# Kernel optimization log

Hardware: AMD Instinct MI355X
Metric: run time of the kernel (lower is better)

Reference implementation:

```python
import jax, jax.numpy as jnp
import numpy as np

TOKENS, D_IN, D_OUT, RANK = 32768, 1024, 1024, 16
SCALE1 = 8.0 / RANK   # alpha=8, rank=16
SCALE2 = 16.0 / RANK  # alpha=16, rank=16


def setup_inputs() -> dict:
    key = jax.random.key(0)
    ks = jax.random.split(key, 7)
    inv = 1.0 / np.sqrt(D_IN)
    return {
        "x": jax.random.normal(ks[0], (TOKENS, D_IN), jnp.float32),
        "W": jax.random.normal(ks[1], (D_OUT, D_IN), jnp.float32) * inv,
        "b": jax.random.normal(ks[2], (D_OUT,), jnp.float32) * 0.01,
        "A1": jax.random.normal(ks[3], (RANK, D_IN), jnp.float32) * inv,
        "B1": jax.random.normal(ks[4], (D_OUT, RANK), jnp.float32) * 0.01,
        "A2": jax.random.normal(ks[5], (RANK, D_IN), jnp.float32) * inv,
        "B2": jax.random.normal(ks[6], (D_OUT, RANK), jnp.float32) * 0.01,
    }


def reference(x, W, b, A1, B1, A2, B2):
    # base linear: [T, D_in] @ [D_in, D_out] + b
    out = jnp.einsum("ti,oi->to", x, W) + b
    # LoRA adapter 1: scale * (x @ A1^T) @ B1^T   (dropout=Identity in eval)
    out = out + SCALE1 * jnp.einsum("tr,or->to", jnp.einsum("ti,ri->tr", x, A1), B1)
    # LoRA adapter 2
    out = out + SCALE2 * jnp.einsum("tr,or->to", jnp.einsum("ti,ri->tr", x, A2), B2)
    return out
```

## Files before the change

### kernel.cpp

```cpp
#include <hip/hip_runtime.h>

#define TOKENS 32768
#define DIN 1024
#define DOUT 1024
#define RANK 16
#define SCALE1 0.5f
#define SCALE2 1.0f

#define BM 128
#define BN 128
#define BK 32

typedef __bf16 bf16x8 __attribute__((ext_vector_type(8)));
typedef float f32x4 __attribute__((ext_vector_type(4)));

__device__ __forceinline__ void load_lds16(const void* gptr, void* lptr) {
    __builtin_amdgcn_global_load_lds(
        (__attribute__((address_space(1))) void*)gptr,
        (__attribute__((address_space(3))) void*)lptr, 16, 0, 0);
}

__global__ void weff_kernel(const float* __restrict__ W, const float* __restrict__ A1,
                            const float* __restrict__ B1, const float* __restrict__ A2,
                            const float* __restrict__ B2, __bf16* __restrict__ Weff) {
    int idx = blockIdx.x * blockDim.x + threadIdx.x;
    int o = idx >> 10;
    int i = idx & 1023;
    float s1 = 0.f, s2 = 0.f;
#pragma unroll
    for (int r = 0; r < RANK; ++r) {
        s1 += B1[o * RANK + r] * A1[r * DIN + i];
        s2 += B2[o * RANK + r] * A2[r * DIN + i];
    }
    Weff[idx] = (__bf16)(W[idx] + SCALE1 * s1 + SCALE2 * s2);
}

__global__ void cvt_x_kernel(const float* __restrict__ x, __bf16* __restrict__ xb) {
    int i = (blockIdx.x * blockDim.x + threadIdx.x) * 8;
    float4 a = *(const float4*)(x + i);
    float4 b = *(const float4*)(x + i + 4);
    bf16x8 v;
    v[0] = (__bf16)a.x; v[1] = (__bf16)a.y; v[2] = (__bf16)a.z; v[3] = (__bf16)a.w;
    v[4] = (__bf16)b.x; v[5] = (__bf16)b.y; v[6] = (__bf16)b.z; v[7] = (__bf16)b.w;
    *(bf16x8*)(xb + i) = v;
}

__global__ __launch_bounds__(256) void gemm_bt_kernel(
    const __bf16* __restrict__ A,
    const __bf16* __restrict__ Bw,
    const float* __restrict__ bias, float* __restrict__ C) {
    __shared__ alignas(16) __bf16 lsA[2][BM * BK];
    __shared__ alignas(16) __bf16 lsB[2][BN * BK];

    const int tid = threadIdx.x;
    const int wave = tid >> 6;
    const int lane = tid & 63;

    const int l = blockIdx.x;
    const int xcd = l & 7;
    const int s = l >> 3;
    const int m0 = (xcd * 32 + (s >> 3)) * BM;
    const int n0 = (s & 7) * BN;

    const int wm = wave >> 1;
    const int wn = wave & 1;

    const int lrow = lane >> 2;
    const int lcol = ((lane & 3) ^ ((lane >> 3) & 3)) * 8;

    const __bf16* gA = A + (size_t)(m0 + wave * 32 + lrow) * DIN + lcol;
    const __bf16* gB = Bw + (size_t)(n0 + wave * 32 + lrow) * DIN + lcol;
    const int so0 = (wave * 32) * BK;
    const int so1 = so0 + 16 * BK;

    f32x4 acc[4][4];
#pragma unroll
    for (int i = 0; i < 4; ++i)
#pragma unroll
        for (int j = 0; j < 4; ++j) acc[i][j] = f32x4{0.f, 0.f, 0.f, 0.f};

    const int fr = lane & 15;
    const int fsw = ((lane >> 4) ^ ((lane >> 1) & 3)) * 8;

    load_lds16(gA, &lsA[0][so0]);
    load_lds16(gA + 16 * DIN, &lsA[0][so1]);
    load_lds16(gB, &lsB[0][so0]);
    load_lds16(gB + 16 * DIN, &lsB[0][so1]);

    int cur = 0;
    for (int k0 = 0; k0 < DIN; k0 += BK) {
        __syncthreads();

        if (k0 + BK < DIN) {
            const int kn = k0 + BK;
            load_lds16(gA + kn, &lsA[cur ^ 1][so0]);
            load_lds16(gA + kn + 16 * DIN, &lsA[cur ^ 1][so1]);
            load_lds16(gB + kn, &lsB[cur ^ 1][so0]);
            load_lds16(gB + kn + 16 * DIN, &lsB[cur ^ 1][so1]);
        }

        bf16x8 af[4], bfv[4];
#pragma unroll
        for (int t = 0; t < 4; ++t) {
            af[t] = *(const bf16x8*)&lsA[cur][(wm * 64 + t * 16 + fr) * BK + fsw];
            bfv[t] = *(const bf16x8*)&lsB[cur][(wn * 64 + t * 16 + fr) * BK + fsw];
        }
#pragma unroll
        for (int mt = 0; mt < 4; ++mt)
#pragma unroll
            for (int nt = 0; nt < 4; ++nt)
                acc[mt][nt] = __builtin_amdgcn_mfma_f32_16x16x32_bf16(
                    af[mt], bfv[nt], acc[mt][nt], 0, 0, 0);
        cur ^= 1;
    }

    const int rbase = (lane >> 4) * 4;
#pragma unroll
    for (int nt = 0; nt < 4; ++nt) {
        const int n = n0 + wn * 64 + nt * 16 + fr;
        const float bv = bias[n];
#pragma unroll
        for (int mt = 0; mt < 4; ++mt) {
            const int m = m0 + wm * 64 + mt * 16 + rbase;
            float* cp = C + (size_t)m * DOUT + n;
#pragma unroll
            for (int r = 0; r < 4; ++r) cp[(size_t)r * DOUT] = acc[mt][nt][r] + bv;
        }
    }
}

extern "C" void kernel_launch(void* const* d_in, const int* in_sizes, int n_in,
                              void* d_out, int out_size, void* d_ws, size_t ws_size,
                              hipStream_t stream) {
    const float* x  = (const float*)d_in[0];
    const float* W  = (const float*)d_in[1];
    const float* b  = (const float*)d_in[2];
    const float* A1 = (const float*)d_in[3];
    const float* B1 = (const float*)d_in[4];
    const float* A2 = (const float*)d_in[5];
    const float* B2 = (const float*)d_in[6];
    float* out = (float*)d_out;

    __bf16* xb   = (__bf16*)d_ws;
    __bf16* Weff = (__bf16*)((char*)d_ws + (size_t)TOKENS * DIN * sizeof(__bf16));

    cvt_x_kernel<<<TOKENS * DIN / (256 * 8), 256, 0, stream>>>(x, xb);
    weff_kernel<<<DOUT * DIN / 256, 256, 0, stream>>>(W, A1, B1, A2, B2, Weff);
    gemm_bt_kernel<<<(TOKENS / BM) * (DOUT / BN), 256, 0, stream>>>(xb, Weff, b, out);
}
```

Before: 330.0 us.

## Use 256x256x64 tiles with 8 waves and phased MFMA/load interleaving

Grows the GEMM block tile to 256x256 with BK=64 and 512 threads (8 waves, each owning a 128x64 sub-tile). The K loop is split into four phases that interleave global-to-LDS prefetch of the next tile with MFMA work, using explicit barriers, setprio and a new 8-column XOR swizzle. The aim is more operand reuse per LDS byte, fewer barriers per FLOP and better overlap of loads with compute. In exchange it uses more registers and LDS per block, which may limit occupancy, and leaves fewer blocks in the grid.

```diff
diff --git a/kernel.cpp b/kernel.cpp
--- a/kernel.cpp
+++ b/kernel.cpp
@@ -7,9 +7,10 @@
 #define SCALE1 0.5f
 #define SCALE2 1.0f
 
-#define BM 128
-#define BN 128
-#define BK 32
+#define BM 256
+#define BN 256
+#define BK 64
+#define KTILES (DIN / BK)
 
 typedef __bf16 bf16x8 __attribute__((ext_vector_type(8)));
 typedef float f32x4 __attribute__((ext_vector_type(4)));
@@ -45,12 +46,12 @@
     *(bf16x8*)(xb + i) = v;
 }
 
-__global__ __launch_bounds__(256) void gemm_bt_kernel(
+__global__ __launch_bounds__(512, 2) void gemm_bt_kernel(
     const __bf16* __restrict__ A,
     const __bf16* __restrict__ Bw,
     const float* __restrict__ bias, float* __restrict__ C) {
-    __shared__ alignas(16) __bf16 lsA[2][BM * BK];
-    __shared__ alignas(16) __bf16 lsB[2][BN * BK];
+    __shared__ alignas(16) __bf16 lsA[2][2][128 * BK];
+    __shared__ alignas(16) __bf16 lsB[2][2][128 * BK];
 
     const int tid = threadIdx.x;
     const int wave = tid >> 6;
@@ -59,69 +60,107 @@
     const int l = blockIdx.x;
     const int xcd = l & 7;
     const int s = l >> 3;
-    const int m0 = (xcd * 32 + (s >> 3)) * BM;
-    const int n0 = (s & 7) * BN;
+    const int m0 = (xcd * 16 + (s >> 2)) * BM;
+    const int n0 = (s & 3) * BN;
 
-    const int wm = wave >> 1;
-    const int wn = wave & 1;
+    const int wm = wave >> 2;
+    const int wn = wave & 3;
 
-    const int lrow = lane >> 2;
-    const int lcol = ((lane & 3) ^ ((lane >> 3) & 3)) * 8;
+    const int srow = lane >> 3;
+    const int scol = ((lane & 7) ^ srow) * 8;
+    const __bf16* gA = A + (size_t)(m0 + wave * 8 + srow) * DIN + scol;
+    const __bf16* gB = Bw + (size_t)(n0 + wave * 8 + srow) * DIN + scol;
+    const int so0 = wave * 512;
+    const int so1 = (8 + wave) * 512;
 
-    const __bf16* gA = A + (size_t)(m0 + wave * 32 + lrow) * DIN + lcol;
-    const __bf16* gB = Bw + (size_t)(n0 + wave * 32 + lrow) * DIN + lcol;
-    const int so0 = (wave * 32) * BK;
-    const int so1 = so0 + 16 * BK;
+#define STAGE_A(buf, kk)                                      \
+    do {                                                      \
+        load_lds16(gA + (kk), &lsA[buf][0][so0]);             \
+        load_lds16(gA + 64 * DIN + (kk), &lsA[buf][0][so1]);  \
+        load_lds16(gA + 128 * DIN + (kk), &lsA[buf][1][so0]); \
+        load_lds16(gA + 192 * DIN + (kk), &lsA[buf][1][so1]); \
+    } while (0)
+#define STAGE_B(buf, kk)                                      \
+    do {                                                      \
+        load_lds16(gB + (kk), &lsB[buf][0][so0]);             \
+        load_lds16(gB + 64 * DIN + (kk), &lsB[buf][0][so1]);  \
+        load_lds16(gB + 128 * DIN + (kk), &lsB[buf][1][so0]); \
+        load_lds16(gB + 192 * DIN + (kk), &lsB[buf][1][so1]); \
+    } while (0)
 
-    f32x4 acc[4][4];
+    const int frow = lane & 15;
+    const int fc0 = ((lane >> 4) ^ (lane & 7)) * 8;
+    const int fc1 = ((4 + (lane >> 4)) ^ (lane & 7)) * 8;
+
+    f32x4 acc[8][4];
 #pragma unroll
-    for (int i = 0; i < 4; ++i)
+    for (int i = 0; i < 8; ++i)
 #pragma unroll
         for (int j = 0; j < 4; ++j) acc[i][j] = f32x4{0.f, 0.f, 0.f, 0.f};
 
-    const int fr = lane & 15;
-    const int fsw = ((lane >> 4) ^ ((lane >> 1) & 3)) * 8;
+    STAGE_A(0, 0);
+    STAGE_B(0, 0);
+    asm volatile("s_waitcnt vmcnt(0)\n\ts_barrier" ::: "memory");
 
-    load_lds16(gA, &lsA[0][so0]);
-    load_lds16(gA + 16 * DIN, &lsA[0][so1]);
-    load_lds16(gB, &lsB[0][so0]);
-    load_lds16(gB + 16 * DIN, &lsB[0][so1]);
-
-    int cur = 0;
-    for (int k0 = 0; k0 < DIN; k0 += BK) {
-        __syncthreads();
-
-        if (k0 + BK < DIN) {
-            const int kn = k0 + BK;
-            load_lds16(gA + kn, &lsA[cur ^ 1][so0]);
-            load_lds16(gA + kn + 16 * DIN, &lsA[cur ^ 1][so1]);
-            load_lds16(gB + kn, &lsB[cur ^ 1][so0]);
-            load_lds16(gB + kn + 16 * DIN, &lsB[cur ^ 1][so1]);
+#pragma unroll 2
+    for (int t = 0; t < KTILES; ++t) {
+        const int cur = t & 1;
+        const int kn = t * BK + BK;
+        const __bf16* baseA = &lsA[cur][wm][0];
+        const __bf16* baseB = &lsB[cur][wn >> 1][(wn & 1) * (64 * BK)];
+#pragma unroll
+        for (int ph = 0; ph < 4; ++ph) {
+            const int mh = ph >> 1;
+            const int nh = ph & 1;
+            bf16x8 af[4][2], bfr[2][2];
+#pragma unroll
+            for (int i = 0; i < 4; ++i) {
+                const int ro = ((mh * 4 + i) * 16 + frow) * BK;
+                af[i][0] = *(const bf16x8*)&baseA[ro + fc0];
+                af[i][1] = *(const bf16x8*)&baseA[ro + fc1];
+            }
+#pragma unroll
+            for (int j = 0; j < 2; ++j) {
+                const int ro = ((nh * 2 + j) * 16 + frow) * BK;
+                bfr[j][0] = *(const bf16x8*)&baseB[ro + fc0];
+                bfr[j][1] = *(const bf16x8*)&baseB[ro + fc1];
+            }
+            if (t < KTILES - 1) {
+                if (ph == 0) STAGE_A(cur ^ 1, kn);
+                if (ph == 1) STAGE_B(cur ^ 1, kn);
+            }
+            asm volatile("s_barrier" ::: "memory");
+            asm volatile("s_waitcnt lgkmcnt(0)" ::: "memory");
+            __builtin_amdgcn_sched_barrier(0);
+            __builtin_amdgcn_s_setprio(1);
+#pragma unroll
+            for (int i = 0; i < 4; ++i)
+#pragma unroll
+                for (int j = 0; j < 2; ++j) {
+                    acc[mh * 4 + i][nh * 2 + j] = __builtin_amdgcn_mfma_f32_16x16x32_bf16(
+                        af[i][0], bfr[j][0], acc[mh * 4 + i][nh * 2 + j], 0, 0, 0);
+                    acc[mh * 4 + i][nh * 2 + j] = __builtin_amdgcn_mfma_f32_16x16x32_bf16(
+                        af[i][1], bfr[j][1], acc[mh * 4 + i][nh * 2 + j], 0, 0, 0);
+                }
+            __builtin_amdgcn_s_setprio(0);
+            if (ph == 3) {
+                asm volatile("s_waitcnt vmcnt(0)\n\ts_barrier" ::: "memory");
+            } else {
+                asm volatile("s_barrier" ::: "memory");
+            }
         }
-
-        bf16x8 af[4], bfv[4];
-#pragma unroll
-        for (int t = 0; t < 4; ++t) {
-            af[t] = *(const bf16x8*)&lsA[cur][(wm * 64 + t * 16 + fr) * BK + fsw];
-            bfv[t] = *(const bf16x8*)&lsB[cur][(wn * 64 + t * 16 + fr) * BK + fsw];
-        }
-#pragma unroll
-        for (int mt = 0; mt < 4; ++mt)
-#pragma unroll
-            for (int nt = 0; nt < 4; ++nt)
-                acc[mt][nt] = __builtin_amdgcn_mfma_f32_16x16x32_bf16(
-                    af[mt], bfv[nt], acc[mt][nt], 0, 0, 0);
-        cur ^= 1;
     }
+#undef STAGE_A
+#undef STAGE_B
 
     const int rbase = (lane >> 4) * 4;
 #pragma unroll
     for (int nt = 0; nt < 4; ++nt) {
-        const int n = n0 + wn * 64 + nt * 16 + fr;
+        const int n = n0 + wn * 64 + nt * 16 + frow;
         const float bv = bias[n];
 #pragma unroll
-        for (int mt = 0; mt < 4; ++mt) {
-            const int m = m0 + wm * 64 + mt * 16 + rbase;
+        for (int mt = 0; mt < 8; ++mt) {
+            const int m = m0 + wm * 128 + mt * 16 + rbase;
             float* cp = C + (size_t)m * DOUT + n;
 #pragma unroll
             for (int r = 0; r < 4; ++r) cp[(size_t)r * DOUT] = acc[mt][nt][r] + bv;
@@ -146,5 +185,5 @@
 
     cvt_x_kernel<<<TOKENS * DIN / (256 * 8), 256, 0, stream>>>(x, xb);
     weff_kernel<<<DOUT * DIN / 256, 256, 0, stream>>>(W, A1, B1, A2, B2, Weff);
-    gemm_bt_kernel<<<(TOKENS / BM) * (DOUT / BN), 256, 0, stream>>>(xb, Weff, b, out);
+    gemm_bt_kernel<<<(TOKENS / BM) * (DOUT / BN), 512, 0, stream>>>(xb, Weff, b, out);
 }
```

New measurement: 333.9 us. About the same (+1.2%).
